# Kernel tuning notes

Hardware: AMD Instinct MI355X
Metric: run time of the kernel (lower is better)

Reference implementation:

```python
import jax, jax.numpy as jnp
import numpy as np

B, D, H, W, C = 2, 8, 64, 64, 128
NH = 8
WS = (2, 8, 8)
SS = (1, 4, 4)
HEAD_DIM = C // NH
SCALE = HEAD_DIM ** -0.5
MLP_HIDDEN = 4 * C


def _window_partition(x, ws):
    # x: (B, D, H, W, C) -> (B*nW, ws0*ws1*ws2, C)
    b, d, h, w, c = x.shape
    x = x.reshape(b, d // ws[0], ws[0], h // ws[1], ws[1], w // ws[2], ws[2], c)
    return x.transpose(0, 1, 3, 5, 2, 4, 6, 7).reshape(-1, ws[0] * ws[1] * ws[2], c)


def _window_reverse(win, ws, b, d, h, w):
    x = win.reshape(b, d // ws[0], h // ws[1], w // ws[2], ws[0], ws[1], ws[2], -1)
    return x.transpose(0, 1, 4, 2, 5, 3, 6, 7).reshape(b, d, h, w, -1)


def _rel_pos_index(ws):
    coords = np.stack(np.meshgrid(np.arange(ws[0]), np.arange(ws[1]), np.arange(ws[2]), indexing='ij'))
    cf = coords.reshape(3, -1)                       # (3, N)
    rel = (cf[:, :, None] - cf[:, None, :]).transpose(1, 2, 0)  # (N, N, 3)
    rel[:, :, 0] += ws[0] - 1
    rel[:, :, 1] += ws[1] - 1
    rel[:, :, 2] += ws[2] - 1
    rel[:, :, 0] *= (2 * ws[1] - 1) * (2 * ws[2] - 1)
    rel[:, :, 1] *= 2 * ws[2] - 1
    return rel.sum(-1)                               # (N, N)


def _attn_mask(d, h, w, ws, ss):
    img = np.zeros((1, d, h, w, 1), np.float32)
    cnt = 0
    for sd in (slice(-ws[0]), slice(-ws[0], -ss[0]), slice(-ss[0], None)):
        for sh in (slice(-ws[1]), slice(-ws[1], -ss[1]), slice(-ss[1], None)):
            for sw in (slice(-ws[2]), slice(-ws[2], -ss[2]), slice(-ss[2], None)):
                img[:, sd, sh, sw, :] = cnt
                cnt += 1
    mw = _window_partition(img, ws)[..., 0]          # (nW, N)
    am = mw[:, None, :] - mw[:, :, None]             # (nW, N, N)
    return np.where(am != 0, -100.0, 0.0).astype(np.float32)


def _ln(x, g, b):
    m = x.mean(-1, keepdims=True)
    v = ((x - m) ** 2).mean(-1, keepdims=True)
    return (x - m) / jnp.sqrt(v + 1e-5) * g + b


def setup_inputs() -> dict:
    key = jax.random.key(0)
    ks = jax.random.split(key, 8)
    n_bias = (2 * WS[0] - 1) * (2 * WS[1] - 1) * (2 * WS[2] - 1)
    return {
        'x': jax.random.normal(ks[0], (B, D, H, W, C), jnp.float32),
        'qkv_w': jax.random.normal(ks[1], (3 * C, C), jnp.float32) * 0.02,
        'qkv_b': jnp.zeros((3 * C,), jnp.float32),
        'proj_w': jax.random.normal(ks[2], (C, C), jnp.float32) * 0.02,
        'proj_b': jnp.zeros((C,), jnp.float32),
        'rpb': jax.random.normal(ks[3], (n_bias, NH), jnp.float32) * 0.02,
        'ln1_g': jnp.ones((C,), jnp.float32),
        'ln1_b': jnp.zeros((C,), jnp.float32),
        'ln2_g': jnp.ones((C,), jnp.float32),
        'ln2_b': jnp.zeros((C,), jnp.float32),
        'fc1_w': jax.random.normal(ks[4], (MLP_HIDDEN, C), jnp.float32) * 0.02,
        'fc1_b': jnp.zeros((MLP_HIDDEN,), jnp.float32),
        'fc2_w': jax.random.normal(ks[5], (C, MLP_HIDDEN), jnp.float32) * 0.02,
        'fc2_b': jnp.zeros((C,), jnp.float32),
    }


def reference(x, qkv_w, qkv_b, proj_w, proj_b, rpb, ln1_g, ln1_b, ln2_g, ln2_b, fc1_w, fc1_b, fc2_w, fc2_b):
    shortcut = x
    xn = _ln(x, ln1_g, ln1_b)
    # cyclic shift (SW-MSA)
    xs = jnp.roll(xn, (-SS[0], -SS[1], -SS[2]), axis=(1, 2, 3))
    win = _window_partition(xs, WS)                  # (Bw, N, C)
    Bw, N, _ = win.shape
    qkv = (win @ qkv_w.T + qkv_b).reshape(Bw, N, 3, NH, HEAD_DIM).transpose(2, 0, 3, 1, 4)
    q, k, v = qkv[0] * SCALE, qkv[1], qkv[2]         # (Bw, NH, N, d)
    attn = jnp.einsum('bhnd,bhmd->bhnm', q, k)       # (Bw, NH, N, N)
    rpi = _rel_pos_index(WS)
    bias = rpb[rpi.reshape(-1)].reshape(N, N, NH).transpose(2, 0, 1)  # (NH, N, N)
    attn = attn + bias[None]
    mask = jnp.asarray(_attn_mask(D, H, W, WS, SS))  # (nW, N, N)
    nW = mask.shape[0]
    attn = attn.reshape(B, nW, NH, N, N) + mask[None, :, None]
    attn = jax.nn.softmax(attn, axis=-1).reshape(Bw, NH, N, N)
    out = jnp.einsum('bhnm,bhmd->bhnd', attn, v).transpose(0, 2, 1, 3).reshape(Bw, N, C)
    out = out @ proj_w.T + proj_b
    xr = _window_reverse(out, WS, B, D, H, W)
    xr = jnp.roll(xr, SS, axis=(1, 2, 3))
    x1 = shortcut + xr
    # MLP block
    y = _ln(x1, ln2_g, ln2_b)
    y = jax.nn.gelu(y @ fc1_w.T + fc1_b, approximate=False)
    y = y @ fc2_w.T + fc2_b
    return x1 + y
```

## Files before the change

### kernel.cpp

```cpp
#include <hip/hip_runtime.h>
#include <math.h>

typedef short s16x8 __attribute__((ext_vector_type(8)));
typedef short s16x4 __attribute__((ext_vector_type(4)));
typedef float f32x4 __attribute__((ext_vector_type(4)));

#define MFMA(a, b, c)    __builtin_amdgcn_mfma_f32_16x16x32_bf16(a, b, c, 0, 0, 0)
#define MFMA16(a, b, c)  __builtin_amdgcn_mfma_f32_16x16x16bf16_1k(a, b, c, 0, 0, 0)

__device__ __forceinline__ float b2f(ushort u) {
    union { unsigned int i; float f; } v; v.i = ((unsigned int)u) << 16; return v.f;
}
__device__ __forceinline__ ushort f2b(float f) {
    union { float f; unsigned int i; } v; v.f = f;
    unsigned int r = v.i + 0x7fffu + ((v.i >> 16) & 1u);
    return (ushort)(r >> 16);
}
__device__ __forceinline__ float gelu_tanh(float v) {
    float u = 0.7978845608f * (v + 0.044715f * v * v * v);
    float e = __expf(-2.f * fabsf(u));
    float t = (1.f - e) / (1.f + e);
    t = (u < 0.f) ? -t : t;
    return 0.5f * v * (1.f + t);
}

__global__ __launch_bounds__(256) void k0_prep(
    const float* __restrict__ qkv_w, const float* __restrict__ proj_w,
    const float* __restrict__ fc1_w, const float* __restrict__ fc2_w,
    const float* __restrict__ rpb, ushort* __restrict__ wq,
    ushort* __restrict__ wp, ushort* __restrict__ wf, ushort* __restrict__ bm)
{
    int bid = blockIdx.x, tid = threadIdx.x;
    if (bid < 192) { int idx = bid * 256 + tid; wq[idx] = f2b(qkv_w[idx]); return; }
    if (bid < 256) { int idx = (bid - 192) * 256 + tid; wp[idx] = f2b(proj_w[idx]); return; }
    if (bid < 768) {
        int idx = (bid - 256) * 256 + tid;
        wf[idx] = f2b(idx < 65536 ? fc1_w[idx] : fc2_w[idx - 65536]);
        return;
    }
    int bi = bid - 768;
    int cls = bi >> 3, head = bi & 7;
    int ed = (cls >> 2) & 1, eh = (cls >> 1) & 1, ew = cls & 1;
    int j = tid & 127;
    int tdj = j >> 6, thj = (j >> 3) & 7, twj = j & 7;
    int regj = (ed ? (tdj + 1) : 0) * 9
             + (eh ? ((thj < 4) ? 1 : 2) : 0) * 3
             + (ew ? ((twj < 4) ? 1 : 2) : 0);
    ushort* bmp = bm + (long)bi * 16384;
    for (int ii = 0; ii < 64; ++ii) {
        int i = (tid >> 7) * 64 + ii;
        int tdi = i >> 6, thi = (i >> 3) & 7, twi = i & 7;
        int regi = (ed ? (tdi + 1) : 0) * 9
                 + (eh ? ((thi < 4) ? 1 : 2) : 0) * 3
                 + (ew ? ((twi < 4) ? 1 : 2) : 0);
        int rpi = (tdi - tdj + 1) * 225 + (thi - thj + 7) * 15 + (twi - twj + 7);
        float v = rpb[rpi * 8 + head] + ((regi != regj) ? -100.f : 0.f);
        bmp[i * 128 + j] = f2b(v);
    }
}

__global__ __launch_bounds__(512) void k23(
    const float* __restrict__ x, const float* __restrict__ g,
    const float* __restrict__ be, const ushort* __restrict__ wq,
    const float* __restrict__ qkv_b, const ushort* __restrict__ bm,
    ushort* __restrict__ obuf)
{
    __shared__ __align__(16) ushort As[128][136];
    __shared__ __align__(16) ushort qb[128][132];
    __shared__ __align__(16) ushort kb[128][132];
    int tid = threadIdx.x;
    int wi = blockIdx.x;
    int wd = (wi >> 6) & 3, wh = (wi >> 3) & 7, ww = wi & 7;
    int cls = ((wd == 3) << 2) | ((wh == 7) << 1) | (ww == 7);
    {
        int row = tid >> 2, part = tid & 3;
        int b = wi >> 8;
        int td = row >> 6, th = (row >> 3) & 7, tw = row & 7;
        int d = (wd * 2 + td + 1) & 7;
        int h = (wh * 8 + th + 4) & 63;
        int w = (ww * 8 + tw + 4) & 63;
        long src = (((long)((b * 8 + d) * 64 + h)) * 64 + w) * 128 + part * 32;
        float vals[32];
        float s = 0.f, q = 0.f;
        #pragma unroll
        for (int i = 0; i < 8; ++i) {
            float4 u = *(const float4*)&x[src + i * 4];
            vals[i * 4 + 0] = u.x; vals[i * 4 + 1] = u.y;
            vals[i * 4 + 2] = u.z; vals[i * 4 + 3] = u.w;
            s += u.x + u.y + u.z + u.w;
            q += u.x * u.x + u.y * u.y + u.z * u.z + u.w * u.w;
        }
        s += __shfl_xor(s, 1); s += __shfl_xor(s, 2);
        q += __shfl_xor(q, 1); q += __shfl_xor(q, 2);
        float mean = s * (1.f / 128.f);
        float rstd = rsqrtf(q * (1.f / 128.f) - mean * mean + 1e-5f);
        #pragma unroll
        for (int i = 0; i < 4; ++i) {
            ushort pk[8];
            #pragma unroll
            for (int jj = 0; jj < 8; ++jj) {
                int c = part * 32 + i * 8 + jj;
                pk[jj] = f2b((vals[i * 8 + jj] - mean) * rstd * g[c] + be[c]);
            }
            *(uint4*)&As[row][part * 32 + i * 8] = *(uint4*)pk;
        }
    }
    __syncthreads();
    int wv = tid >> 6, lane = tid & 63, li = lane & 15, quad = lane >> 4;
    int wm = wv >> 1, wn = wv & 1;
    for (int nb = 0; nb < 3; ++nb) {
        f32x4 acc[2][4] = {};
        for (int s = 0; s < 4; ++s) {
            s16x8 a[2], bw[4];
            #pragma unroll
            for (int mi = 0; mi < 2; ++mi)
                a[mi] = *(const s16x8*)&As[wm * 32 + mi * 16 + li][s * 32 + quad * 8];
            #pragma unroll
            for (int ni = 0; ni < 4; ++ni)
                bw[ni] = *(const s16x8*)&wq[(long)(nb * 128 + wn * 64 + ni * 16 + li) * 128
                                            + s * 32 + quad * 8];
            #pragma unroll
            for (int mi = 0; mi < 2; ++mi)
                #pragma unroll
                for (int ni = 0; ni < 4; ++ni)
                    acc[mi][ni] = MFMA(a[mi], bw[ni], acc[mi][ni]);
        }
        if (nb == 2) __syncthreads();
        #pragma unroll
        for (int mi = 0; mi < 2; ++mi)
            #pragma unroll
            for (int ni = 0; ni < 4; ++ni) {
                int gcol = nb * 128 + wn * 64 + ni * 16 + li;
                float bias = qkv_b[gcol];
                float scale = (nb == 0) ? 0.25f : 1.f;
                #pragma unroll
                for (int r = 0; r < 4; ++r) {
                    int trow = wm * 32 + mi * 16 + quad * 4 + r;
                    ushort val = f2b((acc[mi][ni][r] + bias) * scale);
                    if (nb == 0) {
                        qb[trow][gcol] = val;
                    } else if (nb == 1) {
                        kb[trow][gcol - 128] = val;
                    } else {
                        int c2 = gcol - 256, hh = c2 >> 4, dd = c2 & 15;
                        ((ushort*)As)[hh * 2176 + dd * 136 + trow] = val;
                    }
                }
            }
    }
    __syncthreads();
    const ushort* vtp = (const ushort*)As;
    {
        int h = wv;
        long bmb = (long)(cls * 8 + h) * 16384;
        long ob = (long)wi * 16384 + h * 2048;
        for (int qq = 0; qq < 4; ++qq) {
            int row0 = qq * 32;
            s16x4 qf0 = *(const s16x4*)&qb[row0 + li][h * 16 + quad * 4];
            s16x4 qf1 = *(const s16x4*)&qb[row0 + 16 + li][h * 16 + quad * 4];
            float ps0 = 0.f, ps1 = 0.f;
            uint pa0[8][2], pa1[8][2];
            #pragma unroll
            for (int mi = 0; mi < 8; ++mi) {
                s16x4 kf = *(const s16x4*)&kb[mi * 16 + li][h * 16 + quad * 4];
                f32x4 z = {0.f, 0.f, 0.f, 0.f};
                f32x4 s0 = MFMA16(kf, qf0, z);
                f32x4 s1 = MFMA16(kf, qf1, z);
                s16x4 b0 = *(const s16x4*)&bm[bmb + (row0 + li) * 128 + mi * 16 + quad * 4];
                s16x4 b1 = *(const s16x4*)&bm[bmb + (row0 + 16 + li) * 128 + mi * 16 + quad * 4];
                float e0 = __expf(s0[0] + b2f((ushort)b0[0]));
                float e1 = __expf(s0[1] + b2f((ushort)b0[1]));
                float e2 = __expf(s0[2] + b2f((ushort)b0[2]));
                float e3 = __expf(s0[3] + b2f((ushort)b0[3]));
                ps0 += (e0 + e1) + (e2 + e3);
                pa0[mi][0] = (uint)f2b(e0) | ((uint)f2b(e1) << 16);
                pa0[mi][1] = (uint)f2b(e2) | ((uint)f2b(e3) << 16);
                float f0 = __expf(s1[0] + b2f((ushort)b1[0]));
                float f1 = __expf(s1[1] + b2f((ushort)b1[1]));
                float f2 = __expf(s1[2] + b2f((ushort)b1[2]));
                float f3 = __expf(s1[3] + b2f((ushort)b1[3]));
                ps1 += (f0 + f1) + (f2 + f3);
                pa1[mi][0] = (uint)f2b(f0) | ((uint)f2b(f1) << 16);
                pa1[mi][1] = (uint)f2b(f2) | ((uint)f2b(f3) << 16);
            }
            ps0 += __shfl_xor(ps0, 16); ps0 += __shfl_xor(ps0, 32);
            ps1 += __shfl_xor(ps1, 16); ps1 += __shfl_xor(ps1, 32);
            float inv0 = 1.f / ps0, inv1 = 1.f / ps1;
            f32x4 pc0 = {0.f, 0.f, 0.f, 0.f}, pc1 = {0.f, 0.f, 0.f, 0.f};
            #pragma unroll
            for (int mi = 0; mi < 8; ++mi) {
                s16x4 vf = *(const s16x4*)&vtp[h * 2176 + li * 136 + mi * 16 + quad * 4];
                union { uint2 u; s16x4 v; } a0, a1;
                a0.u.x = pa0[mi][0]; a0.u.y = pa0[mi][1];
                a1.u.x = pa1[mi][0]; a1.u.y = pa1[mi][1];
                pc0 = MFMA16(a0.v, vf, pc0);
                pc1 = MFMA16(a1.v, vf, pc1);
            }
            #pragma unroll
            for (int r = 0; r < 4; ++r) {
                float oi0 = __shfl(inv0, quad * 4 + r);
                float oi1 = __shfl(inv1, quad * 4 + r);
                int i0 = row0 + quad * 4 + r;
                int i1 = row0 + 16 + quad * 4 + r;
                obuf[ob + (long)i0 * 16 + li] = f2b(pc0[r] * oi0);
                obuf[ob + (long)i1 * 16 + li] = f2b(pc1[r] * oi1);
            }
        }
    }
}

__global__ __launch_bounds__(256) void k45(
    const ushort* __restrict__ ao, const ushort* __restrict__ wp,
    const float* __restrict__ proj_b, const float* __restrict__ x,
    const float* __restrict__ g2, const float* __restrict__ be2,
    const ushort* __restrict__ wf1, const float* __restrict__ fc1_b,
    const ushort* __restrict__ wf2, const float* __restrict__ fc2_b,
    float* __restrict__ out)
{
    __shared__ __align__(16) ushort As[64][132];
    __shared__ __align__(16) ushort x1t[64][132];
    __shared__ __align__(16) ushort hs[64][132];
    __shared__ float redS[4][64];
    __shared__ float redQ[4][64];
    int tid = threadIdx.x;
    int b = blockIdx.x;
    int wi = b >> 1, half64 = b & 1;
    int wd = (wi >> 6) & 3, wh = (wi >> 3) & 7, ww = wi & 7;
    int bb = wi >> 8;
    long aob = (long)wi * 16384;
    int tok0 = half64 * 64;
    #pragma unroll
    for (int i = 0; i < 4; ++i) {
        int slot = tid + i * 256;
        int row = slot & 63, hsl = slot >> 6;
        *(uint4*)&As[row][hsl * 8] =
            *(const uint4*)&ao[aob + (hsl >> 1) * 2048 + (long)(tok0 + row) * 16 + (hsl & 1) * 8];
    }
    __syncthreads();
    int wv = tid >> 6, lane = tid & 63, li = lane & 15, quad = lane >> 4;
    int wm = wv >> 1, wn = wv & 1;
    f32x4 acc[2][4] = {};
    for (int s = 0; s < 4; ++s) {
        s16x8 a[2], bw[4];
        #pragma unroll
        for (int mi = 0; mi < 2; ++mi)
            a[mi] = *(const s16x8*)&As[wm * 32 + mi * 16 + li][s * 32 + quad * 8];
        #pragma unroll
        for (int ni = 0; ni < 4; ++ni)
            bw[ni] = *(const s16x8*)&wp[(long)(wn * 64 + ni * 16 + li) * 128 + s * 32 + quad * 8];
        #pragma unroll
        for (int mi = 0; mi < 2; ++mi)
            #pragma unroll
            for (int ni = 0; ni < 4; ++ni)
                acc[mi][ni] = MFMA(a[mi], bw[ni], acc[mi][ni]);
    }
    #pragma unroll
    for (int mi = 0; mi < 2; ++mi) {
        #pragma unroll
        for (int r = 0; r < 4; ++r) {
            int lrow = wm * 32 + mi * 16 + quad * 4 + r;
            int t = half64 * 64 + lrow;
            int td = t >> 6, th = (t >> 3) & 7, tw = t & 7;
            int d = (wd * 2 + td + 1) & 7, h = (wh * 8 + th + 4) & 63, w = (ww * 8 + tw + 4) & 63;
            long di = (((long)((bb * 8 + d) * 64 + h)) * 64 + w) * 128;
            #pragma unroll
            for (int ni = 0; ni < 4; ++ni) {
                int col = wn * 64 + ni * 16 + li;
                x1t[lrow][col] = f2b(acc[mi][ni][r] + proj_b[col] + x[di + col]);
            }
        }
    }
    __syncthreads();
    {
        int token = tid & 63, part = tid >> 6;
        float vals[32];
        float s = 0.f, q = 0.f;
        #pragma unroll
        for (int i = 0; i < 4; ++i) {
            uint4 u = *(const uint4*)&x1t[token][part * 32 + i * 8];
            const ushort* p = (const ushort*)&u;
            #pragma unroll
            for (int j = 0; j < 8; ++j) { float f = b2f(p[j]); vals[i * 8 + j] = f; s += f; q += f * f; }
        }
        redS[part][token] = s; redQ[part][token] = q;
        __syncthreads();
        float st = 0.f, qt = 0.f;
        #pragma unroll
        for (int p2 = 0; p2 < 4; ++p2) { st += redS[p2][token]; qt += redQ[p2][token]; }
        float mean = st * (1.f / 128.f);
        float rstd = rsqrtf(qt * (1.f / 128.f) - mean * mean + 1e-5f);
        #pragma unroll
        for (int i = 0; i < 4; ++i) {
            ushort packed[8];
            #pragma unroll
            for (int j = 0; j < 8; ++j) {
                int c = part * 32 + i * 8 + j;
                packed[j] = f2b((vals[i * 8 + j] - mean) * rstd * g2[c] + be2[c]);
            }
            *(uint4*)&As[token][part * 32 + i * 8] = *(uint4*)packed;
        }
    }
    __syncthreads();
    f32x4 yacc[2][4] = {};
    for (int hc = 0; hc < 4; ++hc) {
        f32x4 hacc[2][4] = {};
        #pragma unroll
        for (int kk = 0; kk < 4; ++kk) {
            s16x8 a[2], bw[4];
            #pragma unroll
            for (int mi = 0; mi < 2; ++mi)
                a[mi] = *(const s16x8*)&As[wm * 32 + mi * 16 + li][kk * 32 + quad * 8];
            #pragma unroll
            for (int ni = 0; ni < 4; ++ni)
                bw[ni] = *(const s16x8*)&wf1[(long)(hc * 128 + wn * 64 + ni * 16 + li) * 128
                                             + kk * 32 + quad * 8];
            #pragma unroll
            for (int mi = 0; mi < 2; ++mi)
                #pragma unroll
                for (int ni = 0; ni < 4; ++ni)
                    hacc[mi][ni] = MFMA(a[mi], bw[ni], hacc[mi][ni]);
        }
        #pragma unroll
        for (int mi = 0; mi < 2; ++mi)
            #pragma unroll
            for (int ni = 0; ni < 4; ++ni) {
                int col = wn * 64 + ni * 16 + li;
                float bbv = fc1_b[hc * 128 + col];
                #pragma unroll
                for (int r = 0; r < 4; ++r) {
                    int row = wm * 32 + mi * 16 + quad * 4 + r;
                    hs[row][col] = f2b(gelu_tanh(hacc[mi][ni][r] + bbv));
                }
            }
        __syncthreads();
        #pragma unroll
        for (int kk = 0; kk < 4; ++kk) {
            s16x8 a[2], bw[4];
            #pragma unroll
            for (int mi = 0; mi < 2; ++mi)
                a[mi] = *(const s16x8*)&hs[wm * 32 + mi * 16 + li][kk * 32 + quad * 8];
            #pragma unroll
            for (int ni = 0; ni < 4; ++ni)
                bw[ni] = *(const s16x8*)&wf2[(long)(wn * 64 + ni * 16 + li) * 512
                                             + hc * 128 + kk * 32 + quad * 8];
            #pragma unroll
            for (int mi = 0; mi < 2; ++mi)
                #pragma unroll
                for (int ni = 0; ni < 4; ++ni)
                    yacc[mi][ni] = MFMA(a[mi], bw[ni], yacc[mi][ni]);
        }
        __syncthreads();
    }
    #pragma unroll
    for (int mi = 0; mi < 2; ++mi) {
        #pragma unroll
        for (int r = 0; r < 4; ++r) {
            int lrow = wm * 32 + mi * 16 + quad * 4 + r;
            int t = half64 * 64 + lrow;
            int td = t >> 6, th = (t >> 3) & 7, tw = t & 7;
            int d = (wd * 2 + td + 1) & 7, h = (wh * 8 + th + 4) & 63, w = (ww * 8 + tw + 4) & 63;
            long di = (((long)((bb * 8 + d) * 64 + h)) * 64 + w) * 128;
            #pragma unroll
            for (int ni = 0; ni < 4; ++ni) {
                int col = wn * 64 + ni * 16 + li;
                out[di + col] = b2f(x1t[lrow][col]) + yacc[mi][ni][r] + fc2_b[col];
            }
        }
    }
}

extern "C" void kernel_launch(void* const* d_in, const int* in_sizes, int n_in,
                              void* d_out, int out_size, void* d_ws, size_t ws_size,
                              hipStream_t stream)
{
    (void)in_sizes; (void)n_in; (void)out_size; (void)ws_size;
    const float* x      = (const float*)d_in[0];
    const float* qkv_w  = (const float*)d_in[1];
    const float* qkv_b  = (const float*)d_in[2];
    const float* proj_w = (const float*)d_in[3];
    const float* proj_b = (const float*)d_in[4];
    const float* rpb    = (const float*)d_in[5];
    const float* ln1_g  = (const float*)d_in[6];
    const float* ln1_b  = (const float*)d_in[7];
    const float* ln2_g  = (const float*)d_in[8];
    const float* ln2_b  = (const float*)d_in[9];
    const float* fc1_w  = (const float*)d_in[10];
    const float* fc1_b  = (const float*)d_in[11];
    const float* fc2_w  = (const float*)d_in[12];
    const float* fc2_b  = (const float*)d_in[13];
    float* out = (float*)d_out;

    ushort* obuf = (ushort*)d_ws;
    ushort* wq   = (ushort*)((char*)d_ws + 50331648);
    ushort* wp   = wq + 49152;
    ushort* wf   = wp + 16384;
    ushort* bm   = wf + 131072;

    hipLaunchKernelGGL(k0_prep, dim3(832), dim3(256), 0, stream,
                       qkv_w, proj_w, fc1_w, fc2_w, rpb, wq, wp, wf, bm);
    hipLaunchKernelGGL(k23, dim3(512), dim3(512), 0, stream,
                       x, ln1_g, ln1_b, wq, qkv_b, bm, obuf);
    hipLaunchKernelGGL(k45, dim3(1024), dim3(256), 0, stream,
                       obuf, wp, proj_b, x, ln2_g, ln2_b,
                       wf, fc1_b, wf + 65536, fc2_b, out);
}
```

Measured before the change: 267.2 us.

## Fuse LN2 stats into proj epilogue, keep residual in registers, double-buffer hs

```diff
diff --git a/kernel.cpp b/kernel.cpp
--- a/kernel.cpp
+++ b/kernel.cpp
@@ -218,10 +218,9 @@
     float* __restrict__ out)
 {
     __shared__ __align__(16) ushort As[64][132];
-    __shared__ __align__(16) ushort x1t[64][132];
-    __shared__ __align__(16) ushort hs[64][132];
-    __shared__ float redS[4][64];
-    __shared__ float redQ[4][64];
+    __shared__ __align__(16) ushort hs[2][64][132];
+    __shared__ float redS[2][64];
+    __shared__ float redQ[2][64];
     int tid = threadIdx.x;
     int b = blockIdx.x;
     int wi = b >> 1, half64 = b & 1;
@@ -254,52 +253,67 @@
             for (int ni = 0; ni < 4; ++ni)
                 acc[mi][ni] = MFMA(a[mi], bw[ni], acc[mi][ni]);
     }
+    int cols[4];
     #pragma unroll
-    for (int mi = 0; mi < 2; ++mi) {
-        #pragma unroll
-        for (int r = 0; r < 4; ++r) {
-            int lrow = wm * 32 + mi * 16 + quad * 4 + r;
-            int t = half64 * 64 + lrow;
-            int td = t >> 6, th = (t >> 3) & 7, tw = t & 7;
-            int d = (wd * 2 + td + 1) & 7, h = (wh * 8 + th + 4) & 63, w = (ww * 8 + tw + 4) & 63;
-            long di = (((long)((bb * 8 + d) * 64 + h)) * 64 + w) * 128;
-            #pragma unroll
-            for (int ni = 0; ni < 4; ++ni) {
-                int col = wn * 64 + ni * 16 + li;
-                x1t[lrow][col] = f2b(acc[mi][ni][r] + proj_b[col] + x[di + col]);
+    for (int ni = 0; ni < 4; ++ni) cols[ni] = wn * 64 + ni * 16 + li;
+    {
+        float pbv[4];
+        #pragma unroll
+        for (int ni = 0; ni < 4; ++ni) pbv[ni] = proj_b[cols[ni]];
+        #pragma unroll
+        for (int mi = 0; mi < 2; ++mi) {
+            #pragma unroll
+            for (int r = 0; r < 4; ++r) {
+                int lrow = wm * 32 + mi * 16 + quad * 4 + r;
+                int t = half64 * 64 + lrow;
+                int td = t >> 6, th = (t >> 3) & 7, tw = t & 7;
+                int d = (wd * 2 + td + 1) & 7, h = (wh * 8 + th + 4) & 63, w = (ww * 8 + tw + 4) & 63;
+                long di = (((long)((bb * 8 + d) * 64 + h)) * 64 + w) * 128;
+                float s_ = 0.f, q_ = 0.f;
+                #pragma unroll
+                for (int ni = 0; ni < 4; ++ni) {
+                    float v = acc[mi][ni][r] + pbv[ni] + x[di + cols[ni]];
+                    acc[mi][ni][r] = v;
+                    s_ += v; q_ += v * v;
+                }
+                #pragma unroll
+                for (int m = 1; m < 16; m <<= 1) {
+                    s_ += __shfl_xor(s_, m);
+                    q_ += __shfl_xor(q_, m);
+                }
+                if (li == 0) { redS[wn][lrow] = s_; redQ[wn][lrow] = q_; }
             }
         }
     }
     __syncthreads();
     {
-        int token = tid & 63, part = tid >> 6;
-        float vals[32];
-        float s = 0.f, q = 0.f;
-        #pragma unroll
-        for (int i = 0; i < 4; ++i) {
-            uint4 u = *(const uint4*)&x1t[token][part * 32 + i * 8];
-            const ushort* p = (const ushort*)&u;
-            #pragma unroll
-            for (int j = 0; j < 8; ++j) { float f = b2f(p[j]); vals[i * 8 + j] = f; s += f; q += f * f; }
-        }
-        redS[part][token] = s; redQ[part][token] = q;
-        __syncthreads();
-        float st = 0.f, qt = 0.f;
-        #pragma unroll
-        for (int p2 = 0; p2 < 4; ++p2) { st += redS[p2][token]; qt += redQ[p2][token]; }
-        float mean = st * (1.f / 128.f);
-        float rstd = rsqrtf(qt * (1.f / 128.f) - mean * mean + 1e-5f);
-        #pragma unroll
-        for (int i = 0; i < 4; ++i) {
-            ushort packed[8];
-            #pragma unroll
-            for (int j = 0; j < 8; ++j) {
-                int c = part * 32 + i * 8 + j;
-                packed[j] = f2b((vals[i * 8 + j] - mean) * rstd * g2[c] + be2[c]);
-            }
-            *(uint4*)&As[token][part * 32 + i * 8] = *(uint4*)packed;
-        }
-    }
+        float g2v[4], be2v[4];
+        #pragma unroll
+        for (int ni = 0; ni < 4; ++ni) { g2v[ni] = g2[cols[ni]]; be2v[ni] = be2[cols[ni]]; }
+        #pragma unroll
+        for (int mi = 0; mi < 2; ++mi) {
+            #pragma unroll
+            for (int r = 0; r < 4; ++r) {
+                int lrow = wm * 32 + mi * 16 + quad * 4 + r;
+                float tS = redS[0][lrow] + redS[1][lrow];
+                float tQ = redQ[0][lrow] + redQ[1][lrow];
+                float mean = tS * (1.f / 128.f);
+                float rstd = rsqrtf(tQ * (1.f / 128.f) - mean * mean + 1e-5f);
+                #pragma unroll
+                for (int ni = 0; ni < 4; ++ni)
+                    As[lrow][cols[ni]] = f2b((acc[mi][ni][r] - mean) * rstd * g2v[ni] + be2v[ni]);
+            }
+        }
+    }
+    uint x1p[2][4][2];
+    #pragma unroll
+    for (int mi = 0; mi < 2; ++mi)
+        #pragma unroll
+        for (int ni = 0; ni < 4; ++ni)
+            #pragma unroll
+            for (int rr = 0; rr < 2; ++rr)
+                x1p[mi][ni][rr] = (unsigned int)f2b(acc[mi][ni][2 * rr])
+                                | ((unsigned int)f2b(acc[mi][ni][2 * rr + 1]) << 16);
     __syncthreads();
     f32x4 yacc[2][4] = {};
     for (int hc = 0; hc < 4; ++hc) {
@@ -329,7 +343,7 @@
                 #pragma unroll
                 for (int r = 0; r < 4; ++r) {
                     int row = wm * 32 + mi * 16 + quad * 4 + r;
-                    hs[row][col] = f2b(gelu_tanh(hacc[mi][ni][r] + bbv));
+                    hs[hc & 1][row][col] = f2b(gelu_tanh(hacc[mi][ni][r] + bbv));
                 }
             }
         __syncthreads();
@@ -338,7 +352,7 @@
             s16x8 a[2], bw[4];
             #pragma unroll
             for (int mi = 0; mi < 2; ++mi)
-                a[mi] = *(const s16x8*)&hs[wm * 32 + mi * 16 + li][kk * 32 + quad * 8];
+                a[mi] = *(const s16x8*)&hs[hc & 1][wm * 32 + mi * 16 + li][kk * 32 + quad * 8];
             #pragma unroll
             for (int ni = 0; ni < 4; ++ni)
                 bw[ni] = *(const s16x8*)&wf2[(long)(wn * 64 + ni * 16 + li) * 512
@@ -349,21 +363,26 @@
                 for (int ni = 0; ni < 4; ++ni)
                     yacc[mi][ni] = MFMA(a[mi], bw[ni], yacc[mi][ni]);
         }
-        __syncthreads();
-    }
-    #pragma unroll
-    for (int mi = 0; mi < 2; ++mi) {
-        #pragma unroll
-        for (int r = 0; r < 4; ++r) {
-            int lrow = wm * 32 + mi * 16 + quad * 4 + r;
-            int t = half64 * 64 + lrow;
-            int td = t >> 6, th = (t >> 3) & 7, tw = t & 7;
-            int d = (wd * 2 + td + 1) & 7, h = (wh * 8 + th + 4) & 63, w = (ww * 8 + tw + 4) & 63;
-            long di = (((long)((bb * 8 + d) * 64 + h)) * 64 + w) * 128;
-            #pragma unroll
-            for (int ni = 0; ni < 4; ++ni) {
-                int col = wn * 64 + ni * 16 + li;
-                out[di + col] = b2f(x1t[lrow][col]) + yacc[mi][ni][r] + fc2_b[col];
+    }
+    {
+        float f2v[4];
+        #pragma unroll
+        for (int ni = 0; ni < 4; ++ni) f2v[ni] = fc2_b[cols[ni]];
+        #pragma unroll
+        for (int mi = 0; mi < 2; ++mi) {
+            #pragma unroll
+            for (int r = 0; r < 4; ++r) {
+                int lrow = wm * 32 + mi * 16 + quad * 4 + r;
+                int t = half64 * 64 + lrow;
+                int td = t >> 6, th = (t >> 3) & 7, tw = t & 7;
+                int d = (wd * 2 + td + 1) & 7, h = (wh * 8 + th + 4) & 63, w = (ww * 8 + tw + 4) & 63;
+                long di = (((long)((bb * 8 + d) * 64 + h)) * 64 + w) * 128;
+                #pragma unroll
+                for (int ni = 0; ni < 4; ++ni) {
+                    unsigned int wrd = x1p[mi][ni][r >> 1];
+                    float x1v = b2f((ushort)((wrd >> ((r & 1) * 16)) & 0xffffu));
+                    out[di + cols[ni]] = x1v + yacc[mi][ni][r] + f2v[ni];
+                }
             }
         }
     }
```

After: 274.6 us. 2.8% more time.
